# Optimization experiments

Hardware: AMD Instinct MI355X
Metric: run time of the kernel (lower is better)

## Reference

```python
import jax, jax.numpy as jnp
import numpy as np

D_MODEL = 2048
N_HEADS = 32
N_KV_HEADS = 8
ROPE_BASE = 10000.0


def setup_inputs() -> dict:
    key = jax.random.key(0)
    ks = jax.random.split(key, 5)
    b, s, d = 2, 2048, D_MODEL
    hd = d // N_HEADS
    scale = 0.02
    return {
        "x": jax.random.normal(ks[0], (b, s, d), jnp.float32),
        "wq": jax.random.normal(ks[1], (N_HEADS * hd, d), jnp.float32) * scale,
        "wk": jax.random.normal(ks[2], (N_KV_HEADS * hd, d), jnp.float32) * scale,
        "wv": jax.random.normal(ks[3], (N_KV_HEADS * hd, d), jnp.float32) * scale,
        "wo": jax.random.normal(ks[4], (d, N_HEADS * hd), jnp.float32) * scale,
    }


def _rope_cos_sin(seq_len, head_dim):
    # theta_j = base^(-2j/d); freqs[i, j] = i * theta_j; repeat-interleave x2 on last dim
    theta = 1.0 / (ROPE_BASE ** (jnp.arange(0, head_dim, 2, dtype=jnp.float32) / head_dim))
    freqs = jnp.arange(seq_len, dtype=jnp.float32)[:, None] * theta[None, :]  # [S, hd/2]
    cos = jnp.repeat(jnp.cos(freqs), 2, axis=-1)[None, :, None, :]  # [1, S, 1, hd]
    sin = jnp.repeat(jnp.sin(freqs), 2, axis=-1)[None, :, None, :]
    return cos, sin


def _rotate(t):
    # interleaved rotate-half: (x0, x1, x2, x3, ...) -> (-x1, x0, -x3, x2, ...)
    t1 = t[..., ::2]
    t2 = t[..., 1::2]
    return jnp.stack([-t2, t1], axis=-1).reshape(t.shape)


def reference(x, wq, wk, wv, wo):
    b, s, d = x.shape
    hd = d // N_HEADS
    n_rep = N_HEADS // N_KV_HEADS

    q = (x @ wq.T).reshape(b, s, N_HEADS, hd)       # [b, s, H, hd]
    k = (x @ wk.T).reshape(b, s, N_KV_HEADS, hd)    # [b, s, G, hd]
    v = (x @ wv.T).reshape(b, s, N_KV_HEADS, hd)

    cos, sin = _rope_cos_sin(s, hd)
    q = q * cos + _rotate(q) * sin
    k = k * cos + _rotate(k) * sin

    # GQA without physical KV replication: group query heads by shared KV head.
    # repeat_interleave(n_rep, dim=2) maps kv head g -> query heads [g*n_rep, (g+1)*n_rep)
    qg = q.reshape(b, s, N_KV_HEADS, n_rep, hd)
    scale = 1.0 / jnp.sqrt(jnp.asarray(hd, q.dtype))
    scores = jnp.einsum('bqgrd,bkgd->bgrqk', qg, k) * scale  # [b, G, rep, Sq, Sk]

    causal = jnp.tril(jnp.ones((s, s), dtype=bool))
    scores = jnp.where(causal[None, None, None], scores, jnp.asarray(-jnp.inf, scores.dtype))
    attn = jax.nn.softmax(scores, axis=-1)

    out = jnp.einsum('bgrqk,bkgd->bqgrd', attn, v).reshape(b, s, N_HEADS * hd)
    return out @ wo.T
```

## Files before the change

### kernel.cpp

```cpp
#include <hip/hip_runtime.h>

typedef unsigned short u16;
typedef __attribute__((ext_vector_type(8))) short bf16x8;
typedef __attribute__((ext_vector_type(4))) float f32x4;

#define LOG2E 1.44269504088896340736f

__device__ inline u16 f2b(float f) {
    unsigned int u = __builtin_bit_cast(unsigned int, f);
    unsigned int r = u + 0x7fffu + ((u >> 16) & 1u);
    return (u16)(r >> 16);
}
__device__ inline float b2f(u16 h) {
    unsigned int u = ((unsigned int)h) << 16;
    return __builtin_bit_cast(float, u);
}

#define GLOAD_LDS16(g, l) \
    __builtin_amdgcn_global_load_lds( \
        (const __attribute__((address_space(1))) unsigned int*)(g), \
        (__attribute__((address_space(3))) unsigned int*)(l), 16, 0, 0)

__global__ __launch_bounds__(256) void cast_all(
    const float* __restrict__ x, const float* __restrict__ wq,
    const float* __restrict__ wk, const float* __restrict__ wv,
    const float* __restrict__ wo, u16* __restrict__ xb,
    u16* __restrict__ wqkvb, u16* __restrict__ wob) {
    long i = ((long)blockIdx.x * 256 + threadIdx.x) * 8;
    const float* s;
    u16* d;
    if (i < 8388608)       { s = x  + i;              d = xb + i; }
    else if (i < 12582912) { s = wq + (i - 8388608);  d = wqkvb + (i - 8388608); }
    else if (i < 13631488) { s = wk + (i - 12582912); d = wqkvb + 4194304 + (i - 12582912); }
    else if (i < 14680064) { s = wv + (i - 13631488); d = wqkvb + 5242880 + (i - 13631488); }
    else                   { s = wo + (i - 14680064); d = wob + (i - 14680064); }
    float4 v0 = *(const float4*)s;
    float4 v1 = *(const float4*)(s + 4);
    ushort4 o0 = make_ushort4(f2b(v0.x), f2b(v0.y), f2b(v0.z), f2b(v0.w));
    ushort4 o1 = make_ushort4(f2b(v1.x), f2b(v1.y), f2b(v1.z), f2b(v1.w));
    *(ushort4*)d = o0;
    *(ushort4*)(d + 4) = o1;
}

__global__ __launch_bounds__(256) void rope_vtrans(
    u16* __restrict__ qkv, u16* __restrict__ VT, float qscale) {
    const int S = 2048, RS = 3072;
    int tid = threadIdx.x;
    if (blockIdx.x < 5120) {
        int idx = blockIdx.x * 256 + tid;
        int row = idx / 320;
        int rem = idx - row * 320;
        int head = rem >> 3, chunk = rem & 7;
        int pos = row & 2047;
        int coloff;
        float scale;
        if (head < 32) { coloff = head * 64;               scale = qscale; }
        else           { coloff = 2048 + (head - 32) * 64; scale = 1.0f; }
        u16* p = qkv + (size_t)row * RS + coloff + chunk * 8;
        bf16x8 v = *(bf16x8*)p;
        float t0 = exp2f((float)(chunk * 4) * -0.41524101186092f);
        const float tc[4] = {1.0f, 0.74989420933246f, 0.56234132519035f, 0.42169650342858f};
        float fpos = (float)pos;
        #pragma unroll
        for (int i = 0; i < 4; i++) {
            float f = fpos * (t0 * tc[i]);
            float rev = f * 0.15915494309189535f;
            rev = rev - floorf(rev);
            float sn = __builtin_amdgcn_sinf(rev);
            float cs = __builtin_amdgcn_cosf(rev);
            float e0 = b2f((u16)v[2 * i]), e1 = b2f((u16)v[2 * i + 1]);
            v[2 * i]     = (short)f2b((e0 * cs - e1 * sn) * scale);
            v[2 * i + 1] = (short)f2b((e1 * cs + e0 * sn) * scale);
        }
        *(bf16x8*)p = v;
    } else {
        int bid = blockIdx.x - 5120;
        int st = bid & 31, g = (bid >> 5) & 7, b = bid >> 8;
        __shared__ u16 T[64 * 72];
        for (int c = tid; c < 512; c += 256) {
            int sr = c >> 3, dc = (c & 7) * 8;
            *(bf16x8*)&T[sr * 72 + dc] =
                *(const bf16x8*)(qkv + ((size_t)b * S + st * 64 + sr) * RS + 2560 + g * 64 + dc);
        }
        __syncthreads();
        for (int c = tid; c < 512; c += 256) {
            int d = c >> 3, sc = (c & 7) * 8;
            bf16x8 o;
            #pragma unroll
            for (int j = 0; j < 8; j++) o[j] = (short)T[(sc + j) * 72 + d];
            *(bf16x8*)(VT + ((size_t)((b * 8 + g) * 64 + d)) * S + st * 64 + sc) = o;
        }
    }
}

__global__ __launch_bounds__(256) void gemm_bt128(
    const u16* __restrict__ A, const u16* __restrict__ B, void* __restrict__ Cv,
    int M, int N, int K, int c_is_f32) {
    __shared__ u16 As[128 * 32];
    __shared__ u16 Bs[128 * 32];
    const int tid = threadIdx.x;
    const int lane = tid & 63, wave = tid >> 6;
    const int ln = lane & 15, quad = lane >> 4;
    const int wm = wave >> 1, wn = wave & 1;

    const int gx = gridDim.x;
    const int nwg = gx * gridDim.y;
    const int bid = blockIdx.y * gx + blockIdx.x;
    const int cpx = nwg >> 3;
    const int swz = (bid & 7) * cpx + (bid >> 3);
    const int m0 = (swz / gx) * 128, n0 = (swz % gx) * 128;

    const int srow = wave * 16 + (lane >> 2);
    const int skc = (lane & 3) * 8;
    const u16* Ag = A + (size_t)(m0 + srow) * K + skc;
    const u16* Bg = B + (size_t)(n0 + srow) * K + skc;

    f32x4 acc[4][4] = {};
    for (int k0 = 0; k0 < K; k0 += 32) {
        #pragma unroll
        for (int t = 0; t < 2; t++) {
            GLOAD_LDS16(Ag + (size_t)t * 64 * K + k0, As + t * 2048 + wave * 512);
            GLOAD_LDS16(Bg + (size_t)t * 64 * K + k0, Bs + t * 2048 + wave * 512);
        }
        __syncthreads();

        bf16x8 af[4], bfr[4];
        #pragma unroll
        for (int i = 0; i < 4; i++) {
            af[i]  = *(const bf16x8*)&As[(wm * 64 + i * 16 + ln) * 32 + quad * 8];
            bfr[i] = *(const bf16x8*)&Bs[(wn * 64 + i * 16 + ln) * 32 + quad * 8];
        }
        #pragma unroll
        for (int mi = 0; mi < 4; mi++)
            #pragma unroll
            for (int nt = 0; nt < 4; nt++)
                acc[mi][nt] = __builtin_amdgcn_mfma_f32_16x16x32_bf16(
                    af[mi], bfr[nt], acc[mi][nt], 0, 0, 0);
        __syncthreads();
    }

    #pragma unroll
    for (int mi = 0; mi < 4; mi++)
        #pragma unroll
        for (int nt = 0; nt < 4; nt++)
            #pragma unroll
            for (int r = 0; r < 4; r++) {
                int row = m0 + wm * 64 + mi * 16 + quad * 4 + r;
                int col = n0 + wn * 64 + nt * 16 + ln;
                float v = acc[mi][nt][r];
                if (c_is_f32) ((float*)Cv)[(size_t)row * N + col] = v;
                else          ((u16*)Cv)[(size_t)row * N + col] = f2b(v);
            }
}

__global__ __launch_bounds__(512) void attn_kernel(
    const u16* __restrict__ QKV, const u16* __restrict__ VT, u16* __restrict__ O) {
    const int S = 2048, RS = 3072, DO = 2048;
    const int bid = blockIdx.x;
    const int swz = (bid & 7) * 64 + (bid >> 3);
    const int p = swz & 15, hp = (swz >> 4) & 15, b = swz >> 8;
    const int g = hp >> 1;
    const int qtl = p, qth = 31 - p;
    const int tid = threadIdx.x;
    const int lane = tid & 63, wave = tid >> 6;
    const int hw = wave >> 2, lw = wave & 3;
    const int h = hp * 2 + hw;
    const int ln = lane & 15, quad = lane >> 4;

    __shared__ u16 Ks[2][64 * 64];
    __shared__ u16 Ps[4][64 * 68];
    u16* Psh = &Ps[hw * 2 + 0][0];
    u16* Psl = &Ps[hw * 2 + 1][0];

    const u16* Qb = QKV + (size_t)b * S * RS + h * 64 + quad * 8;
    bf16x8 aqh0 = *(const bf16x8*)(Qb + (size_t)(qth * 64 + lw * 16 + ln) * RS);
    bf16x8 aqh1 = *(const bf16x8*)(Qb + (size_t)(qth * 64 + lw * 16 + ln) * RS + 32);
    bf16x8 aql0 = *(const bf16x8*)(Qb + (size_t)(qtl * 64 + lw * 16 + ln) * RS);
    bf16x8 aql1 = *(const bf16x8*)(Qb + (size_t)(qtl * 64 + lw * 16 + ln) * RS + 32);

    const u16* Kb = QKV + (size_t)b * S * RS + 2048 + g * 64;
    const u16* VTb = VT + (size_t)(b * 8 + g) * 64 * S;

    const bf16x8 vones = {0x3F80, 0x3F80, 0x3F80, 0x3F80, 0x3F80, 0x3F80, 0x3F80, 0x3F80};

    f32x4 acch[5] = {}, accl[5] = {};

    const int kr = tid >> 3;
    const int ks = tid & 7;
    const int kswz = ((ks ^ (kr & 7)) * 8);
    bf16x8 kreg;
    bf16x8 vr[2][4];
    auto loadK = [&](int kt) {
        kreg = *(const bf16x8*)(Kb + (size_t)(kt * 64 + kr) * RS + ks * 8);
    };
    auto loadV = [&](int kt) {
        #pragma unroll
        for (int kk = 0; kk < 2; kk++)
            #pragma unroll
            for (int nt = 0; nt < 4; nt++)
                vr[kk][nt] = *(const bf16x8*)(VTb + (size_t)(nt * 16 + ln) * S
                                              + kt * 64 + kk * 32 + quad * 8);
    };

    auto body = [&](int kt, bool DUAL, bool MH, bool ML) {
        u16* KsC = &Ks[kt & 1][0];
        u16* KsN = &Ks[(kt & 1) ^ 1][0];
        if (kt < qth) {
            *(bf16x8*)&KsN[kr * 64 + kswz] = kreg;
        }
        if (kt + 2 <= qth) loadK(kt + 2);

        const int rsw = ln & 7;
        f32x4 sh[4] = {}, sl[4] = {};
        __builtin_amdgcn_s_setprio(1);
        #pragma unroll
        for (int nt = 0; nt < 4; nt++) {
            bf16x8 bk0 = *(const bf16x8*)&KsC[(nt * 16 + ln) * 64 + ((quad ^ rsw) * 8)];
            bf16x8 bk1 = *(const bf16x8*)&KsC[(nt * 16 + ln) * 64 + (((quad + 4) ^ rsw) * 8)];
            sh[nt] = __builtin_amdgcn_mfma_f32_16x16x32_bf16(aqh0, bk0, sh[nt], 0, 0, 0);
            sh[nt] = __builtin_amdgcn_mfma_f32_16x16x32_bf16(aqh1, bk1, sh[nt], 0, 0, 0);
            if (DUAL) {
                sl[nt] = __builtin_amdgcn_mfma_f32_16x16x32_bf16(aql0, bk0, sl[nt], 0, 0, 0);
                sl[nt] = __builtin_amdgcn_mfma_f32_16x16x32_bf16(aql1, bk1, sl[nt], 0, 0, 0);
            }
        }
        __builtin_amdgcn_s_setprio(0);

        if (MH) {
            #pragma unroll
            for (int nt = 0; nt < 4; nt++)
                #pragma unroll
                for (int r = 0; r < 4; r++)
                    if (nt * 16 + ln > lw * 16 + quad * 4 + r) sh[nt][r] = -INFINITY;
        }
        #pragma unroll
        for (int nt = 0; nt < 4; nt++)
            #pragma unroll
            for (int r = 0; r < 4; r++) {
                float pv = exp2f(sh[nt][r]);
                Psh[(lw * 16 + quad * 4 + r) * 68 + nt * 16 + ln] =
                    (u16)(__builtin_bit_cast(unsigned int, pv) >> 16);
            }
        if (DUAL) {
            if (ML) {
                #pragma unroll
                for (int nt = 0; nt < 4; nt++)
                    #pragma unroll
                    for (int r = 0; r < 4; r++)
                        if (nt * 16 + ln > lw * 16 + quad * 4 + r) sl[nt][r] = -INFINITY;
            }
            #pragma unroll
            for (int nt = 0; nt < 4; nt++)
                #pragma unroll
                for (int r = 0; r < 4; r++) {
                    float pv = exp2f(sl[nt][r]);
                    Psl[(lw * 16 + quad * 4 + r) * 68 + nt * 16 + ln] =
                        (u16)(__builtin_bit_cast(unsigned int, pv) >> 16);
                }
        }

        __builtin_amdgcn_s_setprio(1);
        #pragma unroll
        for (int kk = 0; kk < 2; kk++) {
            bf16x8 aph = *(const bf16x8*)&Psh[(lw * 16 + ln) * 68 + kk * 32 + quad * 8];
            #pragma unroll
            for (int nt = 0; nt < 4; nt++)
                acch[nt] = __builtin_amdgcn_mfma_f32_16x16x32_bf16(aph, vr[kk][nt], acch[nt], 0, 0, 0);
            acch[4] = __builtin_amdgcn_mfma_f32_16x16x32_bf16(aph, vones, acch[4], 0, 0, 0);
            if (DUAL) {
                bf16x8 apl = *(const bf16x8*)&Psl[(lw * 16 + ln) * 68 + kk * 32 + quad * 8];
                #pragma unroll
                for (int nt = 0; nt < 4; nt++)
                    accl[nt] = __builtin_amdgcn_mfma_f32_16x16x32_bf16(apl, vr[kk][nt], accl[nt], 0, 0, 0);
                accl[4] = __builtin_amdgcn_mfma_f32_16x16x32_bf16(apl, vones, accl[4], 0, 0, 0);
            }
        }
        __builtin_amdgcn_s_setprio(0);

        if (kt < qth) loadV(kt + 1);
        __syncthreads();
    };

    loadK(0);
    loadV(0);
    *(bf16x8*)&Ks[0][kr * 64 + kswz] = kreg;
    loadK(1);
    __syncthreads();

    for (int kt = 0; kt < qtl; kt++) body(kt, true, false, false);
    body(qtl, true, false, true);
    for (int kt = qtl + 1; kt < qth; kt++) body(kt, false, false, false);
    body(qth, false, true, false);

    u16* Ob = O + (size_t)b * S * DO + h * 64;
    #pragma unroll
    for (int r = 0; r < 4; r++) {
        float invh = 1.0f / acch[4][r];
        float invl = 1.0f / accl[4][r];
        int qh = qth * 64 + lw * 16 + quad * 4 + r;
        int ql = qtl * 64 + lw * 16 + quad * 4 + r;
        #pragma unroll
        for (int nt = 0; nt < 4; nt++) {
            Ob[(size_t)qh * DO + nt * 16 + ln] = f2b(acch[nt][r] * invh);
            Ob[(size_t)ql * DO + nt * 16 + ln] = f2b(accl[nt][r] * invl);
        }
    }
}

extern "C" void kernel_launch(void* const* d_in, const int* in_sizes, int n_in,
                              void* d_out, int out_size, void* d_ws, size_t ws_size,
                              hipStream_t stream) {
    const float* x  = (const float*)d_in[0];
    const float* wq = (const float*)d_in[1];
    const float* wk = (const float*)d_in[2];
    const float* wv = (const float*)d_in[3];
    const float* wo = (const float*)d_in[4];

    const int B = 2, S = 2048, D = 2048, H = 32, KVH = 8;
    const int M = B * S;
    const int NQKV = 3072;

    char* ws = (char*)d_ws;
    size_t off = 0;
    auto alloc = [&](size_t bytes) {
        void* p = ws + off;
        off += (bytes + 255) & ~(size_t)255;
        return p;
    };
    u16* xb    = (u16*)alloc((size_t)M * D * 2);
    u16* wqkvb = (u16*)alloc((size_t)NQKV * D * 2);
    u16* wob   = (u16*)alloc((size_t)D * D * 2);
    u16* QKV   = (u16*)alloc((size_t)M * NQKV * 2);
    u16* AO = xb;
    u16* VT = wqkvb;

    cast_all<<<dim3(9216), 256, 0, stream>>>(x, wq, wk, wv, wo, xb, wqkvb, wob);

    gemm_bt128<<<dim3(NQKV / 128, M / 128), 256, 0, stream>>>(xb, wqkvb, QKV, M, NQKV, D, 0);

    const float sscale = 0.125f * LOG2E;
    rope_vtrans<<<dim3(5632), 256, 0, stream>>>(QKV, VT, sscale);

    attn_kernel<<<dim3(512), 512, 0, stream>>>(QKV, VT, AO);

    gemm_bt128<<<dim3(D / 128, M / 128), 256, 0, stream>>>(AO, wob, d_out, M, D, D, 1);
}
```

Before: 372.9 us.

## Replace 128x128 GEMM with 256x256 double-buffered, swizzled-LDS pipelined GEMM

Swaps the simple 128x128 bf16 MFMA GEMM for a 256x256 tile kernel with 8 waves. LDS is double-buffered with XOR-swizzled layout, and global-to-LDS loads for the next k-tile are interleaved with four MFMA quadrants under explicit barriers, waitcnts and setprio. The aim is to hide memory latency, raise arithmetic intensity per tile and cut LDS bank conflicts. In exchange, far fewer workgroups are launched (192 and 128), which may underfill the CUs, and the kernel uses much more LDS and many more registers.

Measured after the change: 365.9 us. About the same (-1.9%).

```diff
diff --git a/kernel.cpp b/kernel.cpp
--- a/kernel.cpp
+++ b/kernel.cpp
@@ -93,61 +93,127 @@
     }
 }
 
-__global__ __launch_bounds__(256) void gemm_bt128(
+#define MMAQ(MH, NH, AR, BR) do { \
+    __builtin_amdgcn_s_setprio(1); \
+    _Pragma("unroll") \
+    for (int m2 = 0; m2 < 4; m2++) { \
+        _Pragma("unroll") \
+        for (int n2 = 0; n2 < 2; n2++) { \
+            acc[(MH)*4+m2][(NH)*2+n2] = __builtin_amdgcn_mfma_f32_16x16x32_bf16( \
+                AR[m2][0], BR[n2][0], acc[(MH)*4+m2][(NH)*2+n2], 0, 0, 0); \
+            acc[(MH)*4+m2][(NH)*2+n2] = __builtin_amdgcn_mfma_f32_16x16x32_bf16( \
+                AR[m2][1], BR[n2][1], acc[(MH)*4+m2][(NH)*2+n2], 0, 0, 0); \
+        } \
+    } \
+    __builtin_amdgcn_s_setprio(0); \
+} while (0)
+
+#define BAR()    do { __builtin_amdgcn_s_barrier(); \
+                      __builtin_amdgcn_sched_barrier(0); } while (0)
+#define LGKM0()  do { asm volatile("s_waitcnt lgkmcnt(0)" ::: "memory"); \
+                      __builtin_amdgcn_sched_barrier(0); } while (0)
+#define VMCNT(n) do { asm volatile("s_waitcnt vmcnt(" #n ")" ::: "memory"); \
+                      __builtin_amdgcn_sched_barrier(0); } while (0)
+
+__global__ __launch_bounds__(512) void gemm_bt256(
     const u16* __restrict__ A, const u16* __restrict__ B, void* __restrict__ Cv,
     int M, int N, int K, int c_is_f32) {
-    __shared__ u16 As[128 * 32];
-    __shared__ u16 Bs[128 * 32];
+    __shared__ u16 As[32768];
+    __shared__ u16 Bs[32768];
     const int tid = threadIdx.x;
-    const int lane = tid & 63, wave = tid >> 6;
+    const int w = tid >> 6, lane = tid & 63;
     const int ln = lane & 15, quad = lane >> 4;
-    const int wm = wave >> 1, wn = wave & 1;
+    const int wr = w >> 2, wc = w & 3;
 
     const int gx = gridDim.x;
     const int nwg = gx * gridDim.y;
     const int bid = blockIdx.y * gx + blockIdx.x;
     const int cpx = nwg >> 3;
     const int swz = (bid & 7) * cpx + (bid >> 3);
-    const int m0 = (swz / gx) * 128, n0 = (swz % gx) * 128;
-
-    const int srow = wave * 16 + (lane >> 2);
-    const int skc = (lane & 3) * 8;
-    const u16* Ag = A + (size_t)(m0 + srow) * K + skc;
-    const u16* Bg = B + (size_t)(n0 + srow) * K + skc;
-
-    f32x4 acc[4][4] = {};
-    for (int k0 = 0; k0 < K; k0 += 32) {
-        #pragma unroll
-        for (int t = 0; t < 2; t++) {
-            GLOAD_LDS16(Ag + (size_t)t * 64 * K + k0, As + t * 2048 + wave * 512);
-            GLOAD_LDS16(Bg + (size_t)t * 64 * K + k0, Bs + t * 2048 + wave * 512);
-        }
-        __syncthreads();
-
-        bf16x8 af[4], bfr[4];
-        #pragma unroll
-        for (int i = 0; i < 4; i++) {
-            af[i]  = *(const bf16x8*)&As[(wm * 64 + i * 16 + ln) * 32 + quad * 8];
-            bfr[i] = *(const bf16x8*)&Bs[(wn * 64 + i * 16 + ln) * 32 + quad * 8];
-        }
-        #pragma unroll
-        for (int mi = 0; mi < 4; mi++)
-            #pragma unroll
-            for (int nt = 0; nt < 4; nt++)
-                acc[mi][nt] = __builtin_amdgcn_mfma_f32_16x16x32_bf16(
-                    af[mi], bfr[nt], acc[mi][nt], 0, 0, 0);
-        __syncthreads();
+    const int m0 = (swz / gx) * 256, n0 = (swz % gx) * 256;
+
+    const int l3 = lane >> 3, l7 = lane & 7;
+    const u16* Ast = A + (size_t)(m0 + w * 8 + l3) * K + (l7 ^ l3) * 8;
+    const u16* Bst = B + (size_t)(n0 + w * 8 + l3) * K + (l7 ^ l3) * 8;
+
+    auto stageA = [&](int u, int h) {
+        const u16* g = Ast + (size_t)(h * 128) * K + u * 64;
+        u16* d = As + ((u & 1) * 2 + h) * 8192 + w * 512;
+        GLOAD_LDS16(g, d);
+        GLOAD_LDS16(g + (size_t)64 * K, d + 4096);
+    };
+    auto stageB = [&](int u, int h) {
+        const u16* g = Bst + (size_t)(h * 128) * K + u * 64;
+        u16* d = Bs + ((u & 1) * 2 + h) * 8192 + w * 512;
+        GLOAD_LDS16(g, d);
+        GLOAD_LDS16(g + (size_t)64 * K, d + 4096);
+    };
+
+    const int xs0 = ((quad) ^ (ln & 7)) * 8;
+    const int xs1 = ((4 + quad) ^ (ln & 7)) * 8;
+
+    bf16x8 a[4][2], b0[2][2], b1[2][2];
+    auto loadA = [&](int u, int mh, bf16x8 (&dst)[4][2]) {
+        const u16* base = As + ((u & 1) * 2 + wr) * 8192 + (mh * 64 + ln) * 64;
+        #pragma unroll
+        for (int m2 = 0; m2 < 4; m2++) {
+            dst[m2][0] = *(const bf16x8*)(base + m2 * 1024 + xs0);
+            dst[m2][1] = *(const bf16x8*)(base + m2 * 1024 + xs1);
+        }
+    };
+    auto loadB = [&](int u, int nh, bf16x8 (&dst)[2][2]) {
+        const u16* base = Bs + ((u & 1) * 2 + (wc >> 1)) * 8192
+                        + ((wc & 1) * 64 + nh * 32 + ln) * 64;
+        #pragma unroll
+        for (int n2 = 0; n2 < 2; n2++) {
+            dst[n2][0] = *(const bf16x8*)(base + n2 * 1024 + xs0);
+            dst[n2][1] = *(const bf16x8*)(base + n2 * 1024 + xs1);
+        }
+    };
+
+    f32x4 acc[8][4] = {};
+    const int NT = K >> 6;
+
+    stageB(0, 0); stageB(0, 1);
+    stageA(0, 0); stageA(0, 1);
+    stageB(1, 0); stageB(1, 1);
+    VMCNT(4);
+    BAR();
+
+    for (int u = 0; u < NT; ++u) {
+        loadA(u, 0, a);
+        loadB(u, 0, b0);
+        if (u + 1 < NT) stageA(u + 1, 0);
+        BAR(); LGKM0();
+        MMAQ(0, 0, a, b0);
+        BAR();
+        loadB(u, 1, b1);
+        if (u + 1 < NT) stageA(u + 1, 1);
+        BAR(); LGKM0();
+        MMAQ(0, 1, a, b1);
+        BAR();
+        loadA(u, 1, a);
+        if (u + 2 < NT) stageB(u + 2, 0);
+        BAR(); LGKM0();
+        MMAQ(1, 1, a, b1);
+        BAR();
+        if (u + 2 < NT) stageB(u + 2, 1);
+        BAR();
+        MMAQ(1, 0, a, b0);
+        if (u + 2 < NT)      { VMCNT(4); }
+        else if (u + 1 < NT) { VMCNT(0); }
+        BAR();
     }
 
     #pragma unroll
-    for (int mi = 0; mi < 4; mi++)
-        #pragma unroll
-        for (int nt = 0; nt < 4; nt++)
+    for (int mi = 0; mi < 8; mi++)
+        #pragma unroll
+        for (int ni = 0; ni < 4; ni++)
             #pragma unroll
             for (int r = 0; r < 4; r++) {
-                int row = m0 + wm * 64 + mi * 16 + quad * 4 + r;
-                int col = n0 + wn * 64 + nt * 16 + ln;
-                float v = acc[mi][nt][r];
+                int row = m0 + wr * 128 + mi * 16 + quad * 4 + r;
+                int col = n0 + wc * 64 + ni * 16 + ln;
+                float v = acc[mi][ni][r];
                 if (c_is_f32) ((float*)Cv)[(size_t)row * N + col] = v;
                 else          ((u16*)Cv)[(size_t)row * N + col] = f2b(v);
             }
@@ -316,7 +382,7 @@
     const float* wv = (const float*)d_in[3];
     const float* wo = (const float*)d_in[4];
 
-    const int B = 2, S = 2048, D = 2048, H = 32, KVH = 8;
+    const int B = 2, S = 2048, D = 2048;
     const int M = B * S;
     const int NQKV = 3072;
 
@@ -336,12 +402,12 @@
 
     cast_all<<<dim3(9216), 256, 0, stream>>>(x, wq, wk, wv, wo, xb, wqkvb, wob);
 
-    gemm_bt128<<<dim3(NQKV / 128, M / 128), 256, 0, stream>>>(xb, wqkvb, QKV, M, NQKV, D, 0);
+    gemm_bt256<<<dim3(NQKV / 256, M / 256), 512, 0, stream>>>(xb, wqkvb, QKV, M, NQKV, D, 0);
 
     const float sscale = 0.125f * LOG2E;
     rope_vtrans<<<dim3(5632), 256, 0, stream>>>(QKV, VT, sscale);
 
     attn_kernel<<<dim3(512), 512, 0, stream>>>(QKV, VT, AO);
 
-    gemm_bt128<<<dim3(D / 128, M / 128), 256, 0, stream>>>(AO, wob, d_out, M, D, D, 1);
-}
+    gemm_bt256<<<dim3(D / 256, M / 256), 512, 0, stream>>>(AO, wob, d_out, M, D, D, 1);
+}
```
